# Optimization experiments

Hardware: AMD Instinct MI355X
Metric: run time of the kernel (lower is better)

## Reference

```python
import jax, jax.numpy as jnp
import numpy as np

B, S, D = 2, 2048, 2048
NH, NKV = 32, 8
HD = D // NH           # 64
GS = NH // NKV         # 4
ROPE_BASE = 10000.0


def _rope_tables(seq_len, head_dim, base):
    inv_freq = 1.0 / (base ** (jnp.arange(head_dim // 2, dtype=jnp.float32) / (head_dim // 2)))
    angles = jnp.arange(seq_len, dtype=jnp.float32)[:, None] * inv_freq[None, :]  # [S, HD/2]
    angles = jnp.concatenate([angles, angles], axis=-1)                            # [S, HD]
    return jnp.cos(angles), jnp.sin(angles)


def _apply_rope(x, cos, sin):
    # x: [B, H, S, HD]
    hd = x.shape[-1]
    x1, x2 = x[..., : hd // 2], x[..., hd // 2 :]
    rotated = jnp.concatenate([-x2, x1], axis=-1)
    return (x * cos[None, None] + rotated * sin[None, None]).astype(x.dtype)


def setup_inputs() -> dict:
    key = jax.random.key(0)
    ks = jax.random.split(key, 5)
    scale = 0.02
    return {
        "x": jax.random.normal(ks[0], (B, S, D), dtype=jnp.float32),
        "Wq": jax.random.normal(ks[1], (D, D), dtype=jnp.float32) * scale,
        "Wk": jax.random.normal(ks[2], (D, NKV * HD), dtype=jnp.float32) * scale,
        "Wv": jax.random.normal(ks[3], (D, NKV * HD), dtype=jnp.float32) * scale,
        "Wo": jax.random.normal(ks[4], (D, D), dtype=jnp.float32) * scale,
    }


def reference(x, Wq, Wk, Wv, Wo):
    b, n, _ = x.shape
    cos, sin = _rope_tables(n, HD, ROPE_BASE)

    q = (x @ Wq).reshape(b, n, NH, HD).transpose(0, 2, 1, 3)    # [B, NH, S, HD]
    k = (x @ Wk).reshape(b, n, NKV, HD).transpose(0, 2, 1, 3)   # [B, NKV, S, HD]
    v = (x @ Wv).reshape(b, n, NKV, HD).transpose(0, 2, 1, 3)

    q = _apply_rope(q, cos, sin)
    k = _apply_rope(k, cos, sin)

    # GQA head sharing: repeat_interleave KV groups to full head count
    k = jnp.repeat(k, GS, axis=1)   # [B, NH, S, HD]
    v = jnp.repeat(v, GS, axis=1)

    scores = jnp.einsum("bhqd,bhkd->bhqk", q, k)                # [B, NH, S, S]
    causal = jnp.triu(jnp.ones((n, n), dtype=bool), k=1)
    scores = jnp.where(causal[None, None], -jnp.inf, scores)
    weights = jax.nn.softmax(scores / jnp.sqrt(jnp.float32(HD)), axis=-1)

    ctx = jnp.einsum("bhqk,bhkd->bhqd", weights, v)             # [B, NH, S, HD]
    ctx = ctx.transpose(0, 2, 1, 3).reshape(b, n, D)
    return ctx @ Wo
```

## Files before the change

kernel.cpp:

```cpp
#include <hip/hip_runtime.h>

typedef __bf16 bf16;
typedef __attribute__((ext_vector_type(8))) __bf16 bf16x8;
typedef __attribute__((ext_vector_type(4))) float f32x4;
typedef __attribute__((ext_vector_type(4))) short s16x4;

#define S_LEN 2048
#define D_MODEL 2048
#define NHEADS 32
#define NKVH 8
#define HDIM 64
#define BATCH 2

__device__ __forceinline__ void async_cp16(const bf16* g, bf16* l) {
    __builtin_amdgcn_global_load_lds(
        (const __attribute__((address_space(1))) unsigned int*)g,
        (__attribute__((address_space(3))) unsigned int*)l, 16, 0, 0);
}

__global__ void cvt_f32_bf16(const float* __restrict__ in, bf16* __restrict__ out, int n4) {
    int i = blockIdx.x * blockDim.x + threadIdx.x;
    if (i < n4) {
        float4 f = ((const float4*)in)[i];
        union { bf16 h[4]; uint2 u; } t;
        t.h[0] = (bf16)f.x; t.h[1] = (bf16)f.y; t.h[2] = (bf16)f.z; t.h[3] = (bf16)f.w;
        ((uint2*)out)[i] = t.u;
    }
}

__global__ void transpose_w(const float* __restrict__ W, bf16* __restrict__ Wt, int K, int N) {
    __shared__ float tile[32][33];
    int kt = blockIdx.y * 32, nt = blockIdx.x * 32;
    int tx = threadIdx.x, ty = threadIdx.y;
    #pragma unroll
    for (int i = 0; i < 32; i += 8)
        tile[ty + i][tx] = W[(size_t)(kt + ty + i) * N + nt + tx];
    __syncthreads();
    #pragma unroll
    for (int i = 0; i < 32; i += 8)
        Wt[(size_t)(nt + ty + i) * K + kt + tx] = (bf16)tile[tx][ty + i];
}

__global__ void transpose_v(const bf16* __restrict__ QKV, bf16* __restrict__ Vt) {
    __shared__ bf16 tl[32][33];
    int z = blockIdx.z;
    int s0 = blockIdx.x * 32, d0 = blockIdx.y * 32;
    int bb = z >> 3, hh = z & 7;
    int tx = threadIdx.x, ty = threadIdx.y;
    #pragma unroll
    for (int i = 0; i < 32; i += 8)
        tl[ty + i][tx] = QKV[((size_t)(bb * S_LEN + s0 + ty + i)) * 3072 + 2560 + hh * 64 + d0 + tx];
    __syncthreads();
    #pragma unroll
    for (int i = 0; i < 32; i += 8)
        Vt[((size_t)z * 64 + d0 + ty + i) * S_LEN + s0 + tx] = tl[tx][ty + i];
}

#define BUF1 16384

#define VMW(n) asm volatile("s_waitcnt vmcnt(" #n ")" ::: "memory")

#define STAGE_A0(BUFOFF) do { \
    async_cp16(pa00, As + (BUFOFF) + la00); \
    async_cp16(pa01, As + (BUFOFF) + la01); \
    pa00 += 64; pa01 += 64; } while (0)
#define STAGE_A1(BUFOFF) do { \
    async_cp16(pa10, As + (BUFOFF) + la10); \
    async_cp16(pa11, As + (BUFOFF) + la11); \
    pa10 += 64; pa11 += 64; } while (0)
#define STAGE_B0(BUFOFF) do { \
    async_cp16(pb00, Bs + (BUFOFF) + lb00); \
    async_cp16(pb01, Bs + (BUFOFF) + lb01); \
    pb00 += 64; pb01 += 64; } while (0)
#define STAGE_B1(BUFOFF) do { \
    async_cp16(pb10, Bs + (BUFOFF) + lb10); \
    async_cp16(pb11, Bs + (BUFOFF) + lb11); \
    pb10 += 64; pb11 += 64; } while (0)

#define READ_A(QM, BUFOFF) do { \
    _Pragma("unroll") \
    for (int m_ = 0; m_ < 4; ++m_) { \
        const int row_ = wr * 128 + (QM) * 64 + m_ * 16 + l16; \
        af[m_][0] = *(const bf16x8*)&As[(BUFOFF) + row_ * 64 + ((quad ^ sw8) * 8)]; \
        af[m_][1] = *(const bf16x8*)&As[(BUFOFF) + row_ * 64 + (((4 + quad) ^ sw8) * 8)]; \
    } } while (0)

#define READ_B(QN, BUFOFF) do { \
    _Pragma("unroll") \
    for (int n_ = 0; n_ < 2; ++n_) { \
        const int row_ = wc * 64 + (QN) * 32 + n_ * 16 + l16; \
        bfr[n_][0] = *(const bf16x8*)&Bs[(BUFOFF) + row_ * 64 + ((quad ^ sw8) * 8)]; \
        bfr[n_][1] = *(const bf16x8*)&Bs[(BUFOFF) + row_ * 64 + (((4 + quad) ^ sw8) * 8)]; \
    } } while (0)

#define MFMA_Q(QM, QN) do { \
    _Pragma("unroll") \
    for (int kk_ = 0; kk_ < 2; ++kk_) \
        _Pragma("unroll") \
        for (int m_ = 0; m_ < 4; ++m_) \
            _Pragma("unroll") \
            for (int n_ = 0; n_ < 2; ++n_) \
                acc[(QM) * 4 + m_][(QN) * 2 + n_] = __builtin_amdgcn_mfma_f32_16x16x32_bf16( \
                    af[m_][kk_], bfr[n_][kk_], acc[(QM) * 4 + m_][(QN) * 2 + n_], 0, 0, 0); \
    } while (0)

#define SYNC_MFMA(QM, QN) do { \
    __builtin_amdgcn_s_barrier(); \
    asm volatile("s_waitcnt lgkmcnt(0)" ::: "memory"); \
    __builtin_amdgcn_sched_barrier(0); \
    __builtin_amdgcn_s_setprio(1); \
    MFMA_Q(QM, QN); \
    __builtin_amdgcn_s_setprio(0); } while (0)

#define TILE4(CUR, S1, S2, S3, S4, WAIT) \
    READ_A(0, CUR); READ_B(0, CUR); S1; SYNC_MFMA(0, 0); __builtin_amdgcn_s_barrier(); \
    READ_B(1, CUR);                 S2; SYNC_MFMA(0, 1); __builtin_amdgcn_s_barrier(); \
    READ_A(1, CUR); READ_B(0, CUR); S3; SYNC_MFMA(1, 0); __builtin_amdgcn_s_barrier(); \
    READ_B(1, CUR);                 S4; SYNC_MFMA(1, 1); WAIT; __builtin_amdgcn_s_barrier();

template <bool OUT_BF16>
__global__ __launch_bounds__(512, 2) void gemm256(const bf16* __restrict__ A,
                                                  const bf16* __restrict__ Bt,
                                                  void* __restrict__ Cv,
                                                  int N, int K) {
    __shared__ __align__(16) bf16 As[2 * 256 * 64];
    __shared__ __align__(16) bf16 Bs[2 * 256 * 64];

    const int tid  = threadIdx.x;
    const int w    = tid >> 6;
    const int lane = tid & 63;
    const int l16  = lane & 15;
    const int quad = lane >> 4;
    const int sw8  = l16 & 7;
    const int wr   = w >> 2;
    const int wc   = w & 3;

    const int nbx  = N >> 8;
    const int nwg  = gridDim.x;
    const int orig = blockIdx.x;
    const int wg   = (orig & 7) * (nwg >> 3) + (orig >> 3);
    const int n0   = (wg % nbx) * 256;
    const int m0   = (wg / nbx) * 256;

    const int krow = lane >> 3;
    const int kc   = (lane & 7) ^ krow;

    const bf16* pa00 = A + (size_t)(m0 +   0 + w * 8 + krow) * K + kc * 8;
    const bf16* pa01 = A + (size_t)(m0 + 128 + w * 8 + krow) * K + kc * 8;
    const bf16* pa10 = A + (size_t)(m0 +  64 + w * 8 + krow) * K + kc * 8;
    const bf16* pa11 = A + (size_t)(m0 + 192 + w * 8 + krow) * K + kc * 8;
    const int brow0 = (w >> 2) * 64 + (w & 3) * 8 + krow;
    const bf16* pb00 = Bt + (size_t)(n0 +       brow0) * K + kc * 8;
    const bf16* pb01 = Bt + (size_t)(n0 + 128 + brow0) * K + kc * 8;
    const bf16* pb10 = Bt + (size_t)(n0 +  32 + brow0) * K + kc * 8;
    const bf16* pb11 = Bt + (size_t)(n0 + 160 + brow0) * K + kc * 8;

    const int la00 = w * 512;
    const int la01 = 8192 + w * 512;
    const int la10 = 4096 + w * 512;
    const int la11 = 12288 + w * 512;
    const int lbb  = ((w >> 2) * 64 + (w & 3) * 8) * 64;
    const int lb00 = lbb;
    const int lb01 = 8192 + lbb;
    const int lb10 = 2048 + lbb;
    const int lb11 = 10240 + lbb;

    f32x4 acc[8][4];
    #pragma unroll
    for (int i = 0; i < 8; ++i)
        #pragma unroll
        for (int j = 0; j < 4; ++j) acc[i][j] = (f32x4){0.f, 0.f, 0.f, 0.f};

    bf16x8 af[4][2];
    bf16x8 bfr[2][2];

    STAGE_A0(0); STAGE_B0(0); STAGE_A1(0); STAGE_B1(0);
    STAGE_A0(BUF1); STAGE_B0(BUF1);
    VMW(4);
    __builtin_amdgcn_s_barrier();

    const int NITER = K >> 7;
    for (int it = 0; it < NITER - 1; ++it) {
        TILE4(0,    STAGE_A1(BUF1), STAGE_B1(BUF1), STAGE_A0(0),    STAGE_B0(0),    VMW(4))
        TILE4(BUF1, STAGE_A1(0),    STAGE_B1(0),    STAGE_A0(BUF1), STAGE_B0(BUF1), VMW(4))
    }
    TILE4(0,    STAGE_A1(BUF1), STAGE_B1(BUF1), , , VMW(0))
    TILE4(BUF1, , , , , )

    #pragma unroll
    for (int mi = 0; mi < 8; ++mi)
        #pragma unroll
        for (int ni = 0; ni < 4; ++ni)
            #pragma unroll
            for (int r = 0; r < 4; ++r) {
                size_t row = (size_t)(m0 + wr * 128 + mi * 16 + quad * 4 + r);
                size_t col = (size_t)(n0 + wc * 64 + ni * 16 + l16);
                if (OUT_BF16) ((bf16*)Cv)[row * N + col] = (bf16)acc[mi][ni][r];
                else          ((float*)Cv)[row * N + col] = acc[mi][ni][r];
            }
}

__global__ void rope_relayout(const bf16* __restrict__ QKV,
                              bf16* __restrict__ Qr, bf16* __restrict__ Kr) {
    const int QN = BATCH * S_LEN * NHEADS * 32;
    const int KN = BATCH * S_LEN * NKVH * 32;
    const float LC = 0.28782313662425572f;
    int idx = blockIdx.x * 256 + threadIdx.x;
    if (idx < QN) {
        int j = idx & 31, hh = (idx >> 5) & 31, s = (idx >> 10) & 2047, bb = idx >> 21;
        size_t src = ((size_t)(bb * S_LEN + s)) * 3072 + hh * HDIM + j;
        float x1 = (float)QKV[src], x2 = (float)QKV[src + 32];
        float ang = (float)s * __expf(-(float)j * LC);
        float sn, cs; sincosf(ang, &sn, &cs);
        size_t dst = ((size_t)((bb * NHEADS + hh) * S_LEN + s)) * HDIM + j;
        Qr[dst]      = (bf16)((x1 * cs - x2 * sn) * 0.125f);
        Qr[dst + 32] = (bf16)((x2 * cs + x1 * sn) * 0.125f);
    } else if (idx < QN + KN) {
        int t = idx - QN;
        int j = t & 31, hh = (t >> 5) & 7, s = (t >> 8) & 2047, bb = t >> 19;
        size_t src = ((size_t)(bb * S_LEN + s)) * 3072 + 2048 + hh * HDIM + j;
        float x1 = (float)QKV[src], x2 = (float)QKV[src + 32];
        float ang = (float)s * __expf(-(float)j * LC);
        float sn, cs; sincosf(ang, &sn, &cs);
        size_t dst = ((size_t)((bb * NKVH + hh) * S_LEN + s)) * HDIM + j;
        Kr[dst]      = (bf16)(x1 * cs - x2 * sn);
        Kr[dst + 32] = (bf16)(x2 * cs + x1 * sn);
    }
}

__global__ __launch_bounds__(256, 3) void attn_kernel(const bf16* __restrict__ Q,
                                                      const bf16* __restrict__ K,
                                                      const bf16* __restrict__ Vt,
                                                      bf16* __restrict__ Ctx) {
    __shared__ __align__(16) bf16 KsL[128 * 64];
    __shared__ __align__(16) bf16 VtL[64 * 128];

    static const signed char QTAB[16] = {15,14,13,12, 10,11,8,9, 5,4,7,6, 0,1,2,3};
    const int bx = blockIdx.x;
    const int qt = QTAB[((bx >> 8) << 2) | ((bx >> 6) & 3)];
    const int bh = bx & 63;
    const int b  = bh >> 5;
    const int h  = bh & 31;
    const int kvh = h >> 2;
    const int tid = threadIdx.x;
    const int wave = tid >> 6;
    const int lane = tid & 63;
    const int l16  = lane & 15;
    const int quad = lane >> 4;

    const bf16* Qb = Q  + ((size_t)(b * NHEADS + h)) * S_LEN * HDIM;
    const bf16* Kb = K  + ((size_t)(b * NKVH + kvh)) * S_LEN * HDIM;
    const bf16* Vb = Vt + ((size_t)(b * NKVH + kvh)) * HDIM * S_LEN;

    const int q0 = qt * 128;

    bf16x8 aq[2][2];
    #pragma unroll
    for (int qf = 0; qf < 2; ++qf)
        #pragma unroll
        for (int ks = 0; ks < 2; ++ks)
            aq[qf][ks] = *(const bf16x8*)(Qb + (size_t)(q0 + wave * 32 + qf * 16 + l16) * HDIM + ks * 32 + quad * 8);

    f32x4 O[2][4];
    float M0 = -1e30f, M1 = -1e30f;
    float l0 = 0.f, l1 = 0.f;
    #pragma unroll
    for (int qf = 0; qf < 2; ++qf)
        #pragma unroll
        for (int df = 0; df < 4; ++df) O[qf][df] = (f32x4){0.f,0.f,0.f,0.f};

    const int krow = lane >> 3, kslot = lane & 7;
    const int kc   = kslot ^ (krow & 7);
    const int vslot = lane & 15, vsub = lane >> 4;

    #pragma unroll 1
    for (int kt = 0; kt <= qt; ++kt) {
        const int k0 = kt * 128;
        __syncthreads();
        #pragma unroll
        for (int j = 0; j < 4; ++j) {
            int rbase = (wave * 4 + j) * 8;
            async_cp16(Kb + (size_t)(k0 + rbase + krow) * HDIM + kc * 8, &KsL[rbase * 64]);
            int d0 = (wave * 4 + j) * 4;
            int vrow = d0 + vsub;
            int vc = vslot ^ (vrow & 15);
            async_cp16(Vb + (size_t)vrow * S_LEN + k0 + vc * 8, &VtL[d0 * 128]);
        }
        __syncthreads();

        f32x4 sc[2][8];
        #pragma unroll
        for (int kf = 0; kf < 8; ++kf) {
            sc[0][kf] = (f32x4){0.f,0.f,0.f,0.f};
            sc[1][kf] = (f32x4){0.f,0.f,0.f,0.f};
            #pragma unroll
            for (int ks = 0; ks < 2; ++ks) {
                bf16x8 bk = *(const bf16x8*)&KsL[(kf * 16 + l16) * 64 + (((ks * 4 + quad) ^ (l16 & 7)) * 8)];
                sc[0][kf] = __builtin_amdgcn_mfma_f32_16x16x32_bf16(bk, aq[0][ks], sc[0][kf], 0, 0, 0);
                sc[1][kf] = __builtin_amdgcn_mfma_f32_16x16x32_bf16(bk, aq[1][ks], sc[1][kf], 0, 0, 0);
            }
        }

        if (kt == qt) {
            #pragma unroll
            for (int kf = 0; kf < 8; ++kf)
                #pragma unroll
                for (int r = 0; r < 4; ++r) {
                    int key = kf * 16 + quad * 4 + r;
                    int qi0 = wave * 32 + l16;
                    if (key > qi0)      sc[0][kf][r] = -1e30f;
                    if (key > qi0 + 16) sc[1][kf][r] = -1e30f;
                }
        }

        float mx0 = sc[0][0][0], mx1 = sc[1][0][0];
        #pragma unroll
        for (int kf = 0; kf < 8; ++kf)
            #pragma unroll
            for (int r = 0; r < 4; ++r) {
                mx0 = fmaxf(mx0, sc[0][kf][r]);
                mx1 = fmaxf(mx1, sc[1][kf][r]);
            }
        mx0 = fmaxf(mx0, __shfl_xor(mx0, 16)); mx0 = fmaxf(mx0, __shfl_xor(mx0, 32));
        mx1 = fmaxf(mx1, __shfl_xor(mx1, 16)); mx1 = fmaxf(mx1, __shfl_xor(mx1, 32));

        float Mn0 = fmaxf(M0, mx0), Mn1 = fmaxf(M1, mx1);
        float a0 = __expf(M0 - Mn0), a1 = __expf(M1 - Mn1);
        M0 = Mn0; M1 = Mn1;
        l0 *= a0; l1 *= a1;

        #pragma unroll
        for (int r = 0; r < 4; ++r) {
            float aO0 = __shfl(a0, quad * 4 + r);
            float aO1 = __shfl(a1, quad * 4 + r);
            #pragma unroll
            for (int df = 0; df < 4; ++df) {
                O[0][df][r] *= aO0;
                O[1][df][r] *= aO1;
            }
        }

        #pragma unroll
        for (int kf = 0; kf < 8; ++kf)
            #pragma unroll
            for (int r = 0; r < 4; ++r) {
                float e0 = __expf(sc[0][kf][r] - M0); sc[0][kf][r] = e0; l0 += e0;
                float e1 = __expf(sc[1][kf][r] - M1); sc[1][kf][r] = e1; l1 += e1;
            }

        #pragma unroll
        for (int kf = 0; kf < 8; ++kf) {
            union { bf16 hh[4]; s16x4 s4; } p0, p1;
            #pragma unroll
            for (int r = 0; r < 4; ++r) {
                p0.hh[r] = (bf16)sc[0][kf][r];
                p1.hh[r] = (bf16)sc[1][kf][r];
            }
            #pragma unroll
            for (int df = 0; df < 4; ++df) {
                s16x4 bv = *(const s16x4*)&VtL[(df * 16 + l16) * 128 +
                                               (((kf * 2 + (quad >> 1)) ^ l16) * 8) + (quad & 1) * 4];
                O[0][df] = __builtin_amdgcn_mfma_f32_16x16x16bf16_1k(p0.s4, bv, O[0][df], 0, 0, 0);
                O[1][df] = __builtin_amdgcn_mfma_f32_16x16x16bf16_1k(p1.s4, bv, O[1][df], 0, 0, 0);
            }
        }
    }

    l0 += __shfl_xor(l0, 16); l0 += __shfl_xor(l0, 32);
    l1 += __shfl_xor(l1, 16); l1 += __shfl_xor(l1, 32);
    #pragma unroll
    for (int r = 0; r < 4; ++r) {
        float inv0 = 1.0f / __shfl(l0, quad * 4 + r);
        float inv1 = 1.0f / __shfl(l1, quad * 4 + r);
        size_t row0 = (size_t)b * S_LEN + q0 + wave * 32 + quad * 4 + r;
        bf16* dst0 = Ctx + row0 * D_MODEL + h * HDIM;
        bf16* dst1 = dst0 + (size_t)16 * D_MODEL;
        #pragma unroll
        for (int df = 0; df < 4; ++df) {
            dst0[df * 16 + l16] = (bf16)(O[0][df][r] * inv0);
            dst1[df * 16 + l16] = (bf16)(O[1][df][r] * inv1);
        }
    }
}

extern "C" void kernel_launch(void* const* d_in, const int* in_sizes, int n_in,
                              void* d_out, int out_size, void* d_ws, size_t ws_size,
                              hipStream_t stream) {
    const float* x  = (const float*)d_in[0];
    const float* Wq = (const float*)d_in[1];
    const float* Wk = (const float*)d_in[2];
    const float* Wv = (const float*)d_in[3];
    const float* Wo = (const float*)d_in[4];

    char* p = (char*)d_ws;
    bf16* X16 = (bf16*)p; p += (size_t)4096 * 2048 * 2;
    bf16* WqT = (bf16*)p; p += (size_t)2048 * 2048 * 2;
    bf16* WkT = (bf16*)p; p += (size_t)512 * 2048 * 2;
    bf16* WvT = (bf16*)p; p += (size_t)512 * 2048 * 2;
    bf16* WoT = (bf16*)p; p += (size_t)2048 * 2048 * 2;
    bf16* QKV = (bf16*)p; p += (size_t)4096 * 3072 * 2;
    bf16* Qr  = (bf16*)p; p += (size_t)4096 * 2048 * 2;
    bf16* Kr  = (bf16*)p; p += (size_t)4096 * 512 * 2;
    bf16* Vt  = (bf16*)p; p += (size_t)16 * 64 * 2048 * 2;
    bf16* Ctx = QKV;

    cvt_f32_bf16<<<8192, 256, 0, stream>>>(x, X16, 2097152);
    transpose_w<<<dim3(64, 64), dim3(32, 8), 0, stream>>>(Wq, WqT, 2048, 2048);
    transpose_w<<<dim3(16, 64), dim3(32, 8), 0, stream>>>(Wk, WkT, 2048, 512);
    transpose_w<<<dim3(16, 64), dim3(32, 8), 0, stream>>>(Wv, WvT, 2048, 512);
    transpose_w<<<dim3(64, 64), dim3(32, 8), 0, stream>>>(Wo, WoT, 2048, 2048);

    gemm256<true><<<dim3(192), 512, 0, stream>>>(X16, WqT, (void*)QKV, 3072, 2048);

    rope_relayout<<<20480, 256, 0, stream>>>(QKV, Qr, Kr);
    transpose_v<<<dim3(64, 2, 16), dim3(32, 8), 0, stream>>>(QKV, Vt);
    attn_kernel<<<1024, 256, 0, stream>>>(Qr, Kr, Vt, Ctx);

    gemm256<false><<<dim3(128), 512, 0, stream>>>(Ctx, WoT, d_out, 2048, 2048);
}
```

Baseline: 321.0 us.

## Restructure GEMM LDS pipeline to refill current buffer and double-buffer B fragments

Reworks the 256x256 GEMM main loop so that each k-tile's async global->LDS loads refill the buffer just consumed, keeping two full k-tiles in flight, instead of split staging across buffers. B fragments are held in two register sets (bfr0/bfr1), so the second half of the tile reuses them without re-reading LDS. The goal is fewer LDS reads and deeper prefetch overlap. In exchange it uses more VGPRs and depends on barrier ordering to avoid overwriting LDS data still being read.

```diff
diff --git a/kernel.cpp b/kernel.cpp
--- a/kernel.cpp
+++ b/kernel.cpp
@@ -59,6 +59,7 @@
 #define BUF1 16384
 
 #define VMW(n) asm volatile("s_waitcnt vmcnt(" #n ")" ::: "memory")
+#define BAR __builtin_amdgcn_s_barrier()
 
 #define STAGE_A0(BUFOFF) do { \
     async_cp16(pa00, As + (BUFOFF) + la00); \
@@ -85,15 +86,15 @@
         af[m_][1] = *(const bf16x8*)&As[(BUFOFF) + row_ * 64 + (((4 + quad) ^ sw8) * 8)]; \
     } } while (0)
 
-#define READ_B(QN, BUFOFF) do { \
+#define READ_B(QN, BUFOFF, BV) do { \
     _Pragma("unroll") \
     for (int n_ = 0; n_ < 2; ++n_) { \
         const int row_ = wc * 64 + (QN) * 32 + n_ * 16 + l16; \
-        bfr[n_][0] = *(const bf16x8*)&Bs[(BUFOFF) + row_ * 64 + ((quad ^ sw8) * 8)]; \
-        bfr[n_][1] = *(const bf16x8*)&Bs[(BUFOFF) + row_ * 64 + (((4 + quad) ^ sw8) * 8)]; \
+        BV[n_][0] = *(const bf16x8*)&Bs[(BUFOFF) + row_ * 64 + ((quad ^ sw8) * 8)]; \
+        BV[n_][1] = *(const bf16x8*)&Bs[(BUFOFF) + row_ * 64 + (((4 + quad) ^ sw8) * 8)]; \
     } } while (0)
 
-#define MFMA_Q(QM, QN) do { \
+#define MFMA_Q(QM, QN, BV) do { \
     _Pragma("unroll") \
     for (int kk_ = 0; kk_ < 2; ++kk_) \
         _Pragma("unroll") \
@@ -101,22 +102,28 @@
             _Pragma("unroll") \
             for (int n_ = 0; n_ < 2; ++n_) \
                 acc[(QM) * 4 + m_][(QN) * 2 + n_] = __builtin_amdgcn_mfma_f32_16x16x32_bf16( \
-                    af[m_][kk_], bfr[n_][kk_], acc[(QM) * 4 + m_][(QN) * 2 + n_], 0, 0, 0); \
+                    af[m_][kk_], BV[n_][kk_], acc[(QM) * 4 + m_][(QN) * 2 + n_], 0, 0, 0); \
     } while (0)
 
-#define SYNC_MFMA(QM, QN) do { \
-    __builtin_amdgcn_s_barrier(); \
+#define SYNCM(QM, QN, BV) do { \
+    BAR; \
     asm volatile("s_waitcnt lgkmcnt(0)" ::: "memory"); \
     __builtin_amdgcn_sched_barrier(0); \
     __builtin_amdgcn_s_setprio(1); \
-    MFMA_Q(QM, QN); \
+    MFMA_Q(QM, QN, BV); \
     __builtin_amdgcn_s_setprio(0); } while (0)
 
-#define TILE4(CUR, S1, S2, S3, S4, WAIT) \
-    READ_A(0, CUR); READ_B(0, CUR); S1; SYNC_MFMA(0, 0); __builtin_amdgcn_s_barrier(); \
-    READ_B(1, CUR);                 S2; SYNC_MFMA(0, 1); __builtin_amdgcn_s_barrier(); \
-    READ_A(1, CUR); READ_B(0, CUR); S3; SYNC_MFMA(1, 0); __builtin_amdgcn_s_barrier(); \
-    READ_B(1, CUR);                 S4; SYNC_MFMA(1, 1); WAIT; __builtin_amdgcn_s_barrier();
+#define TILE_S(CUR) do { \
+    READ_A(0, CUR); READ_B(0, CUR, bfr0);             SYNCM(0, 0, bfr0); BAR; \
+    STAGE_A0(CUR); STAGE_B0(CUR); READ_B(1, CUR, bfr1); SYNCM(0, 1, bfr1); BAR; \
+    STAGE_B1(CUR); READ_A(1, CUR);                    SYNCM(1, 0, bfr0); BAR; \
+    STAGE_A1(CUR);                                    SYNCM(1, 1, bfr1); VMW(8); BAR; } while (0)
+
+#define TILE_N(CUR, W) do { \
+    READ_A(0, CUR); READ_B(0, CUR, bfr0); SYNCM(0, 0, bfr0); BAR; \
+    READ_B(1, CUR, bfr1);                 SYNCM(0, 1, bfr1); BAR; \
+    READ_A(1, CUR);                       SYNCM(1, 0, bfr0); BAR; \
+                                          SYNCM(1, 1, bfr1); W; BAR; } while (0)
 
 template <bool OUT_BF16>
 __global__ __launch_bounds__(512, 2) void gemm256(const bf16* __restrict__ A,
@@ -172,20 +179,21 @@
         for (int j = 0; j < 4; ++j) acc[i][j] = (f32x4){0.f, 0.f, 0.f, 0.f};
 
     bf16x8 af[4][2];
-    bf16x8 bfr[2][2];
-
-    STAGE_A0(0); STAGE_B0(0); STAGE_A1(0); STAGE_B1(0);
-    STAGE_A0(BUF1); STAGE_B0(BUF1);
-    VMW(4);
-    __builtin_amdgcn_s_barrier();
-
-    const int NITER = K >> 7;
-    for (int it = 0; it < NITER - 1; ++it) {
-        TILE4(0,    STAGE_A1(BUF1), STAGE_B1(BUF1), STAGE_A0(0),    STAGE_B0(0),    VMW(4))
-        TILE4(BUF1, STAGE_A1(0),    STAGE_B1(0),    STAGE_A0(BUF1), STAGE_B0(BUF1), VMW(4))
+    bf16x8 bfr0[2][2];
+    bf16x8 bfr1[2][2];
+
+    STAGE_A0(0); STAGE_B0(0); STAGE_B1(0); STAGE_A1(0);
+    STAGE_A0(BUF1); STAGE_B0(BUF1); STAGE_B1(BUF1); STAGE_A1(BUF1);
+    VMW(8);
+    BAR;
+
+    const int NITER = K >> 6;
+    for (int it = 0; it < (NITER - 2) >> 1; ++it) {
+        TILE_S(0);
+        TILE_S(BUF1);
     }
-    TILE4(0,    STAGE_A1(BUF1), STAGE_B1(BUF1), , , VMW(0))
-    TILE4(BUF1, , , , , )
+    TILE_N(0, VMW(0));
+    TILE_N(BUF1, );
 
     #pragma unroll
     for (int mi = 0; mi < 8; ++mi)
```

New measurement: 319.2 us. About the same (-0.5%).
